# Optimization experiments

Measured on AMD Instinct MI355X. Metric: run time of the kernel, lower is better.

Reference implementation:

```python
import jax, jax.numpy as jnp
import numpy as np

B, T, D = 2, 2048, 2048
N, K, H = 16, 8, 128  # num_heads, num_kv_heads, head_dim
SOFTCAP = 50.0
ROPE_BASE = 10000.0


def apply_rope(x, positions):
    # x: [B, L, heads, H], positions: [B, L]
    head_dim = x.shape[-1]
    fraction = 2.0 * jnp.arange(head_dim // 2, dtype=jnp.float32) / head_dim
    timescale = ROPE_BASE ** fraction  # [H/2]
    sinusoid = positions.astype(jnp.float32)[..., None] / timescale  # [B, L, H/2]
    sinusoid = sinusoid[..., None, :]  # [B, L, 1, H/2]
    sin, cos = jnp.sin(sinusoid), jnp.cos(sinusoid)
    first, second = jnp.split(x, 2, axis=-1)
    out = jnp.concatenate([first * cos - second * sin,
                           second * cos + first * sin], axis=-1)
    return out.astype(x.dtype)


def setup_inputs() -> dict:
    key = jax.random.key(0)
    kx, kq, kkv, ko = jax.random.split(key, 4)
    x = jax.random.normal(kx, (B, T, D), dtype=jnp.float32)
    positions = jnp.broadcast_to(jnp.arange(T, dtype=jnp.int32), (B, T))
    attn_mask = jnp.broadcast_to(
        jnp.tril(jnp.ones((T, T), dtype=bool))[None, None], (B, 1, T, T))
    # variance-scaling fan_in init approximated with scaled normals
    w_q = jax.random.normal(kq, (N, D, H), dtype=jnp.float32) / np.sqrt(D)
    w_kv = jax.random.normal(kkv, (2, K, D, H), dtype=jnp.float32) / np.sqrt(D)
    w_out = jax.random.normal(ko, (N, H, D), dtype=jnp.float32) / np.sqrt(N * H)
    return {"x": x, "positions": positions, "attn_mask": attn_mask,
            "w_q": w_q, "w_kv": w_kv, "w_out": w_out}


def reference(x, positions, attn_mask, w_q, w_kv, w_out):
    # QKV projections (GQA: separate q and kv einsums)
    q = jnp.einsum('BTD,NDH->BTNH', x, w_q)        # [B,T,N,H]
    kv = jnp.einsum('BSD,cKDH->cBSKH', x, w_kv)     # [2,B,S,K,H]
    k, v = kv[0], kv[1]
    q = apply_rope(q, positions) * (H ** -0.5)      # rsqrt_head_dim norm
    k = apply_rope(k, positions)
    # GQA grouping: N = K * G
    G = N // K
    qg = q.reshape(B, T, K, G, H)
    logits = jnp.einsum('BTKGH,BSKH->BKGTS', qg, k).astype(jnp.float32)
    logits = jnp.tanh(logits / SOFTCAP) * SOFTCAP   # logits softcap
    big_neg = -2.3819763e+38
    masked = jnp.where(attn_mask[:, :, None, :, :], logits, big_neg)
    probs = jax.nn.softmax(masked, axis=-1).astype(k.dtype)
    encoded = jnp.einsum('BKGTS,BSKH->BTKGH', probs, v).reshape(B, T, N, H)
    return jnp.einsum('BTNH,NHD->BTD', encoded, w_out)
```

## Files before the change

kernel.cpp:

```cpp
#include <hip/hip_runtime.h>
#include <math.h>
#include <stdint.h>


typedef unsigned short u16;
using bf16x8 = __attribute__((ext_vector_type(8))) short;
using f32x4  = __attribute__((ext_vector_type(4))) float;

#define MFMA_BF16(a,b,c) __builtin_amdgcn_mfma_f32_16x16x32_bf16((a),(b),(c),0,0,0)

static __device__ __forceinline__ float b2f(u16 u) {
  union { unsigned int i; float f; } v; v.i = ((unsigned int)u) << 16; return v.f;
}
static __device__ __forceinline__ u16 f2b(float f) {
  union { float f; unsigned int i; } v; v.f = f;
  unsigned int r = v.i + 0x7fffu + ((v.i >> 16) & 1u);
  return (u16)(r >> 16);
}
static __device__ __forceinline__ unsigned pk2(float x0, float x1) {
  union { float f; unsigned u; } a, b;
  a.f = x0; b.f = x1;
  return __builtin_amdgcn_perm(b.u + 0x8000u, a.u + 0x8000u, 0x07060302u);
}
static __device__ __forceinline__ void gload_lds16(const void* g, void* l) {
  __builtin_amdgcn_global_load_lds((__attribute__((address_space(1))) void*)(g),
                                   (__attribute__((address_space(3))) void*)(l),
                                   16, 0, 0);
}

__global__ __launch_bounds__(256) void f32_to_bf16(const float* __restrict__ src,
                                                   u16* __restrict__ dst, int n) {
  const int i = (blockIdx.x * 256 + threadIdx.x) * 4;
  if (i < n) {
    const float4 v = *(const float4*)(src + i);
    ushort4 o;
    o.x = f2b(v.x); o.y = f2b(v.y); o.z = f2b(v.z); o.w = f2b(v.w);
    *(ushort4*)(dst + i) = o;
  }
}

__global__ __launch_bounds__(256) void transpose_f32_bf16(const float* __restrict__ src,
                                                          u16* __restrict__ dst,
                                                          int rows, int cols) {
  __shared__ u16 tile[32][33];
  const int c0 = blockIdx.x * 32;
  const int r0 = blockIdx.y * 32;
  const size_t matoff = (size_t)blockIdx.z * (size_t)rows * (size_t)cols;
  const float* s = src + matoff;
  u16* d = dst + matoff;
  const int tx = threadIdx.x, ty = threadIdx.y;
#pragma unroll
  for (int j = 0; j < 4; ++j)
    tile[ty + j * 8][tx] = f2b(s[(size_t)(r0 + ty + j * 8) * cols + (c0 + tx)]);
  __syncthreads();
#pragma unroll
  for (int j = 0; j < 4; ++j)
    d[(size_t)(c0 + ty + j * 8) * rows + (r0 + tx)] = tile[tx][ty + j * 8];
}

__global__ __launch_bounds__(256) void gemm_qkv(const u16* __restrict__ X,
                                                const u16* __restrict__ wqt,
                                                const u16* __restrict__ wkvt,
                                                u16* __restrict__ qb,
                                                u16* __restrict__ kb,
                                                u16* __restrict__ vtb) {
  __shared__ __align__(16) u16 sA[128 * 32];
  __shared__ __align__(16) u16 sB[128 * 32];
  const int m0 = blockIdx.x * 128;
  const int ct = blockIdx.y;
  const u16* Bt = (ct < 16) ? (wqt + (size_t)ct * 128 * 2048)
                            : (wkvt + (size_t)(ct - 16) * 128 * 2048);
  const int tid = threadIdx.x;
  const int wave = tid >> 6, lane = tid & 63;
  const int wm = wave & 1, wn = wave >> 1;
  const int quad = lane >> 4, l16 = lane & 15;
  const int srow = lane >> 2, sch = lane & 3;

  f32x4 acc[4][4] = {};

  for (int k0 = 0; k0 < 2048; k0 += 32) {
#pragma unroll
    for (int s = 0; s < 2; ++s) {
      const int instr = wave * 2 + s;
      const int row = instr * 16 + srow;
      gload_lds16(X + (size_t)(m0 + row) * 2048 + k0 + sch * 8, (char*)sA + instr * 1024);
      gload_lds16(Bt + (size_t)row * 2048 + k0 + sch * 8, (char*)sB + instr * 1024);
    }
    __syncthreads();
    bf16x8 af[4], bfr[4];
#pragma unroll
    for (int mf = 0; mf < 4; ++mf)
      af[mf] = *(const bf16x8*)(sA + (wm * 64 + mf * 16 + l16) * 32 + quad * 8);
#pragma unroll
    for (int nf = 0; nf < 4; ++nf)
      bfr[nf] = *(const bf16x8*)(sB + (wn * 64 + nf * 16 + l16) * 32 + quad * 8);
#pragma unroll
    for (int mf = 0; mf < 4; ++mf)
#pragma unroll
      for (int nf = 0; nf < 4; ++nf)
        acc[mf][nf] = MFMA_BF16(af[mf], bfr[nf], acc[mf][nf]);
    __syncthreads();
  }

#pragma unroll
  for (int mf = 0; mf < 4; ++mf) {
    const int mm = m0 + wm * 64 + mf * 16 + quad * 4;
    const int b = mm >> 11;
    const int t = mm & 2047;
#pragma unroll
    for (int nf = 0; nf < 4; ++nf) {
      const int h = wn * 64 + nf * 16 + l16;
      if (ct < 16) {
        u16* d = qb + (((size_t)b * 16 + ct) * 2048 + t) * 128 + h;
#pragma unroll
        for (int i = 0; i < 4; ++i) d[(size_t)i * 128] = f2b(acc[mf][nf][i]);
      } else if (ct < 24) {
        u16* d = kb + (((size_t)b * 8 + (ct - 16)) * 2048 + t) * 128 + h;
#pragma unroll
        for (int i = 0; i < 4; ++i) d[(size_t)i * 128] = f2b(acc[mf][nf][i]);
      } else {
        u16* d = vtb + (((size_t)b * 8 + (ct - 24)) * 128 + h) * 2048 + t;
        uint2 pkv;
        pkv.x = (unsigned)f2b(acc[mf][nf][0]) | ((unsigned)f2b(acc[mf][nf][1]) << 16);
        pkv.y = (unsigned)f2b(acc[mf][nf][2]) | ((unsigned)f2b(acc[mf][nf][3]) << 16);
        *(uint2*)d = pkv;
      }
    }
  }
}

__global__ __launch_bounds__(256) void rope_kernel(u16* __restrict__ qb,
                                                   u16* __restrict__ kb,
                                                   const int* __restrict__ pos) {
  const size_t idx = (size_t)blockIdx.x * 256 + threadIdx.x;
  const size_t QP = (size_t)1 << 22;
  u16* p;
  float scale;
  int b, t, j;
  if (idx < QP) {
    j = (int)(idx & 63); t = (int)((idx >> 6) & 2047);
    const int hd = (int)((idx >> 17) & 15); b = (int)(idx >> 21);
    p = qb + (((size_t)b * 16 + hd) * 2048 + t) * 128;
    scale = 0.08838834764831845f;
  } else {
    const size_t r = idx - QP;
    j = (int)(r & 63); t = (int)((r >> 6) & 2047);
    const int hd = (int)((r >> 17) & 7); b = (int)(r >> 20);
    p = kb + (((size_t)b * 8 + hd) * 2048 + t) * 128;
    scale = 1.0f;
  }
  const float fpos = (float)pos[(size_t)b * 2048 + t];
  const float ts = __powf(10000.0f, (float)j * (1.0f / 64.0f));
  const float ang = fpos / ts;
  float sn, cs;
  sincosf(ang, &sn, &cs);
  const float a = b2f(p[j]);
  const float c2 = b2f(p[j + 64]);
  p[j] = f2b((a * cs - c2 * sn) * scale);
  p[j + 64] = f2b((c2 * cs + a * sn) * scale);
}

__global__ __launch_bounds__(256) void attn_fused(const u16* __restrict__ qg,
                                                  const u16* __restrict__ kg,
                                                  const u16* __restrict__ vtg,
                                                  u16* __restrict__ enc) {
  __shared__ __align__(16) char lds[32768];
  char* sK = lds;
  char* sV = lds + 16384;

  const int bid = blockIdx.x;
  const int x = bid & 7;
  const int i6 = bid >> 3;
  const int p = i6 & 15;
  const int head = (i6 >> 4) * 8 + x;
  const int b = head >> 4;
  const int n = head & 15;
  const int kh = n >> 1;

  const u16* qbase = qg + ((size_t)b * 16 + n) * 2048 * 128;
  const u16* kbase = kg + ((size_t)b * 8 + kh) * 2048 * 128;
  const u16* vbase = vtg + ((size_t)b * 8 + kh) * 128 * 2048;

  const int tid = threadIdx.x, wave = tid >> 6, lane = tid & 63;
  const int quad = lane >> 4, l16 = lane & 15;
  const int bp_a0 = ((quad & 1) * 32 + l16) * 4;
  const int bp_a1 = bp_a0 + 64;

  const float L2E = 1.4426950408889634f;
  const float C50 = 72.13475204444817f;
  const float A1 = 1.3333333333e-4f;
  const float A2 = 2.1333333333e-8f;
  const float A3 = 3.4539682540e-12f;

#pragma unroll 1
  for (int pass = 0; pass < 2; ++pass) {
    const int Q = pass ? (31 - p) : p;
    const int tw = Q * 64 + wave * 16;
    const int tlane = tw + l16;

    bf16x8 qf[4];
#pragma unroll
    for (int kf = 0; kf < 4; ++kf)
      qf[kf] = *(const bf16x8*)(qbase + (size_t)tlane * 128 + kf * 32 + quad * 8);

    f32x4 o[8] = {};
    f32x4 lacc = {0.f, 0.f, 0.f, 0.f};

#pragma unroll 1
    for (int si = 0; si <= Q; ++si) {
      const int s0 = si * 64;
      __syncthreads();
#pragma unroll
      for (int r2 = 0; r2 < 4; ++r2) {
        const int idx = r2 * 256 + tid;
        const int kr = idx >> 4, kc = idx & 15;
        *(float4*)(sK + kr * 256 + ((kc ^ (kr & 15)) << 4)) =
            *(const float4*)(kbase + (size_t)(s0 + kr) * 128 + kc * 8);
        const int vr = idx >> 3, vc = idx & 7;
        *(float4*)(sV + vr * 128 + ((vc ^ (vr & 7)) << 4)) =
            *(const float4*)(vbase + (size_t)vr * 2048 + s0 + vc * 8);
      }
      __syncthreads();

      const bool diag = (si == Q);
      const int nfmax = diag ? wave : 3;
      const int kmax = diag ? (wave >> 1) : 1;

      f32x4 sacc[4];
#pragma unroll
      for (int nf = 0; nf < 4; ++nf) {
        if (nf <= nfmax) {
          const int sr = nf * 16 + l16;
          f32x4 a = {0.f, 0.f, 0.f, 0.f};
#pragma unroll
          for (int kf = 0; kf < 4; ++kf) {
            const bf16x8 kfr =
                *(const bf16x8*)(sK + sr * 256 + (((kf * 4 + quad) ^ (sr & 15)) << 4));
            a = MFMA_BF16(kfr, qf[kf], a);
          }
          sacc[nf] = a;
        }
      }

#pragma unroll
      for (int nf = 0; nf < 4; ++nf) {
        if (nf <= nfmax) {
          const f32x4 xv = sacc[nf];
          const f32x4 u = xv * xv;
          f32x4 t = u * (-A3) + A2;
          t = u * t + (-A1);
          t = u * t + 1.0f;
          const f32x4 tc = xv * t;
          f32x4 pv;
#pragma unroll
          for (int i = 0; i < 4; ++i) pv[i] = exp2f(fmaf(tc[i], L2E, -C50));
          if (diag) {
#pragma unroll
            for (int i = 0; i < 4; ++i) {
              const int sg = s0 + nf * 16 + quad * 4 + i;
              if (sg > tlane) pv[i] = 0.0f;
            }
          }
          sacc[nf] = pv;
          lacc += pv;
        }
      }

      unsigned pkd[4][2];
#pragma unroll
      for (int nf = 0; nf < 4; ++nf) {
        if (nf <= nfmax) {
          pkd[nf][0] = pk2(sacc[nf][0], sacc[nf][1]);
          pkd[nf][1] = pk2(sacc[nf][2], sacc[nf][3]);
        } else {
          pkd[nf][0] = 0u; pkd[nf][1] = 0u;
        }
      }

#pragma unroll
      for (int c2 = 0; c2 < 2; ++c2) {
        if (c2 <= kmax) {
          const int lo = (quad >> 1);
          const int dA0 = __builtin_amdgcn_ds_bpermute(bp_a0, (int)pkd[2 * c2][0]);
          const int dB0 = __builtin_amdgcn_ds_bpermute(bp_a0, (int)pkd[2 * c2 + 1][0]);
          const int dA1 = __builtin_amdgcn_ds_bpermute(bp_a0, (int)pkd[2 * c2][1]);
          const int dB1 = __builtin_amdgcn_ds_bpermute(bp_a0, (int)pkd[2 * c2 + 1][1]);
          const int dA2 = __builtin_amdgcn_ds_bpermute(bp_a1, (int)pkd[2 * c2][0]);
          const int dB2 = __builtin_amdgcn_ds_bpermute(bp_a1, (int)pkd[2 * c2 + 1][0]);
          const int dA3 = __builtin_amdgcn_ds_bpermute(bp_a1, (int)pkd[2 * c2][1]);
          const int dB3 = __builtin_amdgcn_ds_bpermute(bp_a1, (int)pkd[2 * c2 + 1][1]);
          union { int d[4]; bf16x8 v; } pb;
          pb.d[0] = lo ? dB0 : dA0;
          pb.d[1] = lo ? dB1 : dA1;
          pb.d[2] = lo ? dB2 : dA2;
          pb.d[3] = lo ? dB3 : dA3;
#pragma unroll
          for (int nfo = 0; nfo < 8; ++nfo) {
            const int hr = nfo * 16 + l16;
            const bf16x8 vb =
                *(const bf16x8*)(sV + hr * 128 + (((c2 * 4 + quad) ^ (hr & 7)) << 4));
            o[nfo] = MFMA_BF16(vb, pb.v, o[nfo]);
          }
        }
      }
    }

    float lsum = lacc[0] + lacc[1] + lacc[2] + lacc[3];
    lsum += __shfl_xor(lsum, 16);
    lsum += __shfl_xor(lsum, 32);
    const float inv = 1.0f / lsum;
    u16* d = enc + (((size_t)b * 2048 + tlane) * 16 + n) * 128 + quad * 4;
#pragma unroll
    for (int nfo = 0; nfo < 8; ++nfo) {
      uint2 st;
      st.x = (unsigned)f2b(o[nfo][0] * inv) | ((unsigned)f2b(o[nfo][1] * inv) << 16);
      st.y = (unsigned)f2b(o[nfo][2] * inv) | ((unsigned)f2b(o[nfo][3] * inv) << 16);
      *(uint2*)(d + nfo * 16) = st;
    }
  }
}

__global__ __launch_bounds__(256) void gemm_out(const u16* __restrict__ A,
                                                const u16* __restrict__ Bt,
                                                float* __restrict__ C) {
  __shared__ __align__(16) u16 sA[128 * 32];
  __shared__ __align__(16) u16 sB[128 * 32];
  const int m0 = blockIdx.x * 128;
  const int n0 = blockIdx.y * 128;
  const int tid = threadIdx.x;
  const int wave = tid >> 6, lane = tid & 63;
  const int wm = wave & 1, wn = wave >> 1;
  const int quad = lane >> 4, l16 = lane & 15;
  const int srow = lane >> 2, sch = lane & 3;

  f32x4 acc[4][4] = {};

  for (int k0 = 0; k0 < 2048; k0 += 32) {
#pragma unroll
    for (int s = 0; s < 2; ++s) {
      const int instr = wave * 2 + s;
      const int row = instr * 16 + srow;
      gload_lds16(A + (size_t)(m0 + row) * 2048 + k0 + sch * 8, (char*)sA + instr * 1024);
      gload_lds16(Bt + (size_t)(n0 + row) * 2048 + k0 + sch * 8, (char*)sB + instr * 1024);
    }
    __syncthreads();
    bf16x8 af[4], bfr[4];
#pragma unroll
    for (int mf = 0; mf < 4; ++mf)
      af[mf] = *(const bf16x8*)(sA + (wm * 64 + mf * 16 + l16) * 32 + quad * 8);
#pragma unroll
    for (int nf = 0; nf < 4; ++nf)
      bfr[nf] = *(const bf16x8*)(sB + (wn * 64 + nf * 16 + l16) * 32 + quad * 8);
#pragma unroll
    for (int mf = 0; mf < 4; ++mf)
#pragma unroll
      for (int nf = 0; nf < 4; ++nf)
        acc[mf][nf] = MFMA_BF16(af[mf], bfr[nf], acc[mf][nf]);
    __syncthreads();
  }

#pragma unroll
  for (int mf = 0; mf < 4; ++mf) {
    const int mm = m0 + wm * 64 + mf * 16 + quad * 4;
#pragma unroll
    for (int nf = 0; nf < 4; ++nf) {
      const int col = n0 + wn * 64 + nf * 16 + l16;
#pragma unroll
      for (int i = 0; i < 4; ++i) C[(size_t)(mm + i) * 2048 + col] = acc[mf][nf][i];
    }
  }
}

extern "C" void kernel_launch(void* const* d_in, const int* in_sizes, int n_in,
                              void* d_out, int out_size, void* d_ws, size_t ws_size,
                              hipStream_t stream) {
  (void)in_sizes; (void)n_in; (void)out_size; (void)ws_size;
  const float* x     = (const float*)d_in[0];
  const int*   posi  = (const int*)d_in[1];
  const float* w_q   = (const float*)d_in[3];
  const float* w_kv  = (const float*)d_in[4];
  const float* w_out = (const float*)d_in[5];
  float* out = (float*)d_out;

  u16* ws = (u16*)d_ws;
  u16* wqt   = ws;
  u16* wkvt  = ws + (size_t)4194304;
  u16* woutt = ws + (size_t)8388608;
  u16* qb    = ws + (size_t)12582912;
  u16* kb    = ws + (size_t)20971520;
  u16* vtb   = ws + (size_t)25165824;
  u16* encb  = ws + (size_t)29360128;
  u16* xb    = encb;

  f32_to_bf16<<<8192, 256, 0, stream>>>(x, xb, 8388608);
  transpose_f32_bf16<<<dim3(4, 64, 16), dim3(32, 8, 1), 0, stream>>>(w_q, wqt, 2048, 128);
  transpose_f32_bf16<<<dim3(4, 64, 16), dim3(32, 8, 1), 0, stream>>>(w_kv, wkvt, 2048, 128);
  transpose_f32_bf16<<<dim3(64, 64, 1), dim3(32, 8, 1), 0, stream>>>(w_out, woutt, 2048, 2048);
  gemm_qkv<<<dim3(32, 32), 256, 0, stream>>>(xb, wqt, wkvt, qb, kb, vtb);
  rope_kernel<<<24576, 256, 0, stream>>>(qb, kb, posi);
  attn_fused<<<512, 256, 0, stream>>>(qb, kb, vtb, encb);
  gemm_out<<<dim3(32, 16), 256, 0, stream>>>(encb, woutt, out);
}
```

Baseline: 407.3 us.

## Fuse prep kernels, deepen GEMM K-tile with XOR-swizzled LDS, vectorize RoPE

Merges the input conversion and the three weight transposes into one prep launch, which removes three kernel launches. Both GEMMs now stage a 64-wide K slice per iteration, with an XOR swizzle on the LDS chunk index to avoid bank conflicts. This halves the number of barriers per K loop and doubles LDS use per block. RoPE now handles two element pairs per thread with 32-bit loads and stores, halving the thread count.

```diff
diff --git a/kernel.cpp b/kernel.cpp
--- a/kernel.cpp
+++ b/kernel.cpp
@@ -28,77 +28,101 @@
                                    16, 0, 0);
 }
 
-__global__ __launch_bounds__(256) void f32_to_bf16(const float* __restrict__ src,
-                                                   u16* __restrict__ dst, int n) {
-  const int i = (blockIdx.x * 256 + threadIdx.x) * 4;
-  if (i < n) {
-    const float4 v = *(const float4*)(src + i);
+__global__ __launch_bounds__(256) void prep(const float* __restrict__ x, u16* __restrict__ xb,
+                                            const float* __restrict__ wq,
+                                            const float* __restrict__ wkv,
+                                            const float* __restrict__ wout,
+                                            u16* __restrict__ wqkvt, u16* __restrict__ woutt) {
+  const int tid = threadIdx.x;
+  int bid = blockIdx.x;
+  if (bid < 8192) {
+    const int i = (bid * 256 + tid) * 4;
+    const float4 v = *(const float4*)(x + i);
     ushort4 o;
     o.x = f2b(v.x); o.y = f2b(v.y); o.z = f2b(v.z); o.w = f2b(v.w);
-    *(ushort4*)(dst + i) = o;
-  }
-}
-
-__global__ __launch_bounds__(256) void transpose_f32_bf16(const float* __restrict__ src,
-                                                          u16* __restrict__ dst,
-                                                          int rows, int cols) {
+    *(ushort4*)(xb + i) = o;
+    return;
+  }
+  bid -= 8192;
+  const float* src;
+  u16* dst;
+  int rows, cols, bx, by;
+  if (bid < 8192) {
+    const int seg = bid >> 12;
+    const int r = bid & 4095;
+    const int mat = r >> 8;
+    bx = (r & 255) & 3;
+    by = (r & 255) >> 2;
+    rows = 2048; cols = 128;
+    src = (seg ? wkv : wq) + (size_t)mat * 2048 * 128;
+    dst = wqkvt + (size_t)(seg * 16 + mat) * 2048 * 128;
+  } else {
+    const int r = bid - 8192;
+    bx = r & 63;
+    by = r >> 6;
+    rows = 2048; cols = 2048;
+    src = wout;
+    dst = woutt;
+  }
   __shared__ u16 tile[32][33];
-  const int c0 = blockIdx.x * 32;
-  const int r0 = blockIdx.y * 32;
-  const size_t matoff = (size_t)blockIdx.z * (size_t)rows * (size_t)cols;
-  const float* s = src + matoff;
-  u16* d = dst + matoff;
-  const int tx = threadIdx.x, ty = threadIdx.y;
+  const int c0 = bx * 32, r0 = by * 32;
+  const int tx = tid & 31, ty = tid >> 5;
 #pragma unroll
   for (int j = 0; j < 4; ++j)
-    tile[ty + j * 8][tx] = f2b(s[(size_t)(r0 + ty + j * 8) * cols + (c0 + tx)]);
+    tile[ty + j * 8][tx] = f2b(src[(size_t)(r0 + ty + j * 8) * cols + (c0 + tx)]);
   __syncthreads();
 #pragma unroll
   for (int j = 0; j < 4; ++j)
-    d[(size_t)(c0 + ty + j * 8) * rows + (r0 + tx)] = tile[tx][ty + j * 8];
+    dst[(size_t)(c0 + ty + j * 8) * rows + (r0 + tx)] = tile[tx][ty + j * 8];
 }
 
 __global__ __launch_bounds__(256) void gemm_qkv(const u16* __restrict__ X,
-                                                const u16* __restrict__ wqt,
-                                                const u16* __restrict__ wkvt,
+                                                const u16* __restrict__ wqkvt,
                                                 u16* __restrict__ qb,
                                                 u16* __restrict__ kb,
                                                 u16* __restrict__ vtb) {
-  __shared__ __align__(16) u16 sA[128 * 32];
-  __shared__ __align__(16) u16 sB[128 * 32];
+  __shared__ __align__(16) u16 sA[128 * 64];
+  __shared__ __align__(16) u16 sB[128 * 64];
   const int m0 = blockIdx.x * 128;
   const int ct = blockIdx.y;
-  const u16* Bt = (ct < 16) ? (wqt + (size_t)ct * 128 * 2048)
-                            : (wkvt + (size_t)(ct - 16) * 128 * 2048);
+  const u16* Bt = wqkvt + (size_t)ct * 128 * 2048;
   const int tid = threadIdx.x;
   const int wave = tid >> 6, lane = tid & 63;
   const int wm = wave & 1, wn = wave >> 1;
   const int quad = lane >> 4, l16 = lane & 15;
-  const int srow = lane >> 2, sch = lane & 3;
+  const int srow = lane >> 3;
+  const int sch = (lane & 7) ^ srow;
 
   f32x4 acc[4][4] = {};
 
-  for (int k0 = 0; k0 < 2048; k0 += 32) {
-#pragma unroll
-    for (int s = 0; s < 2; ++s) {
-      const int instr = wave * 2 + s;
-      const int row = instr * 16 + srow;
+  for (int k0 = 0; k0 < 2048; k0 += 64) {
+#pragma unroll
+    for (int s = 0; s < 4; ++s) {
+      const int instr = wave * 4 + s;
+      const int row = instr * 8 + srow;
       gload_lds16(X + (size_t)(m0 + row) * 2048 + k0 + sch * 8, (char*)sA + instr * 1024);
       gload_lds16(Bt + (size_t)row * 2048 + k0 + sch * 8, (char*)sB + instr * 1024);
     }
     __syncthreads();
-    bf16x8 af[4], bfr[4];
-#pragma unroll
-    for (int mf = 0; mf < 4; ++mf)
-      af[mf] = *(const bf16x8*)(sA + (wm * 64 + mf * 16 + l16) * 32 + quad * 8);
-#pragma unroll
-    for (int nf = 0; nf < 4; ++nf)
-      bfr[nf] = *(const bf16x8*)(sB + (wn * 64 + nf * 16 + l16) * 32 + quad * 8);
-#pragma unroll
-    for (int mf = 0; mf < 4; ++mf)
-#pragma unroll
-      for (int nf = 0; nf < 4; ++nf)
-        acc[mf][nf] = MFMA_BF16(af[mf], bfr[nf], acc[mf][nf]);
+#pragma unroll
+    for (int ks = 0; ks < 2; ++ks) {
+      bf16x8 af[4], bfr[4];
+#pragma unroll
+      for (int mf = 0; mf < 4; ++mf) {
+        const int R = wm * 64 + mf * 16 + l16;
+        af[mf] = *(const bf16x8*)((char*)sA + R * 128 + (((ks * 4 + quad) ^ (R & 7)) << 4));
+      }
+#pragma unroll
+      for (int nf = 0; nf < 4; ++nf) {
+        const int R = wn * 64 + nf * 16 + l16;
+        bfr[nf] = *(const bf16x8*)((char*)sB + R * 128 + (((ks * 4 + quad) ^ (R & 7)) << 4));
+      }
+#pragma unroll
+      for (int mf = 0; mf < 4; ++mf)
+#pragma unroll
+        for (int nf = 0; nf < 4; ++nf)
+          acc[mf][nf] = MFMA_BF16(af[mf], bfr[nf], acc[mf][nf]);
+    }
     __syncthreads();
   }
 
@@ -132,32 +156,40 @@
 __global__ __launch_bounds__(256) void rope_kernel(u16* __restrict__ qb,
                                                    u16* __restrict__ kb,
                                                    const int* __restrict__ pos) {
-  const size_t idx = (size_t)blockIdx.x * 256 + threadIdx.x;
-  const size_t QP = (size_t)1 << 22;
+  const unsigned idx = blockIdx.x * 256 + threadIdx.x;
+  const unsigned QP = 1u << 21;
   u16* p;
   float scale;
-  int b, t, j;
+  int b, t, j2;
   if (idx < QP) {
-    j = (int)(idx & 63); t = (int)((idx >> 6) & 2047);
-    const int hd = (int)((idx >> 17) & 15); b = (int)(idx >> 21);
+    j2 = (int)(idx & 31) * 2; t = (int)((idx >> 5) & 2047);
+    const int hd = (int)((idx >> 16) & 15); b = (int)(idx >> 20);
     p = qb + (((size_t)b * 16 + hd) * 2048 + t) * 128;
     scale = 0.08838834764831845f;
   } else {
-    const size_t r = idx - QP;
-    j = (int)(r & 63); t = (int)((r >> 6) & 2047);
-    const int hd = (int)((r >> 17) & 7); b = (int)(r >> 20);
+    const unsigned r = idx - QP;
+    j2 = (int)(r & 31) * 2; t = (int)((r >> 5) & 2047);
+    const int hd = (int)((r >> 16) & 7); b = (int)(r >> 19);
     p = kb + (((size_t)b * 8 + hd) * 2048 + t) * 128;
     scale = 1.0f;
   }
   const float fpos = (float)pos[(size_t)b * 2048 + t];
-  const float ts = __powf(10000.0f, (float)j * (1.0f / 64.0f));
-  const float ang = fpos / ts;
-  float sn, cs;
-  sincosf(ang, &sn, &cs);
-  const float a = b2f(p[j]);
-  const float c2 = b2f(p[j + 64]);
-  p[j] = f2b((a * cs - c2 * sn) * scale);
-  p[j + 64] = f2b((c2 * cs + a * sn) * scale);
+  const unsigned lo = *(const unsigned*)(p + j2);
+  const unsigned hi = *(const unsigned*)(p + j2 + 64);
+  unsigned olo = 0, ohi = 0;
+#pragma unroll
+  for (int d = 0; d < 2; ++d) {
+    const int j = j2 + d;
+    const float ts = __powf(10000.0f, (float)j * (1.0f / 64.0f));
+    float sn, cs;
+    sincosf(fpos / ts, &sn, &cs);
+    const float a = b2f((u16)((d ? (lo >> 16) : lo) & 0xffffu));
+    const float c2 = b2f((u16)((d ? (hi >> 16) : hi) & 0xffffu));
+    olo |= ((unsigned)f2b((a * cs - c2 * sn) * scale)) << (16 * d);
+    ohi |= ((unsigned)f2b((c2 * cs + a * sn) * scale)) << (16 * d);
+  }
+  *(unsigned*)(p + j2) = olo;
+  *(unsigned*)(p + j2 + 64) = ohi;
 }
 
 __global__ __launch_bounds__(256) void attn_fused(const u16* __restrict__ qg,
@@ -323,39 +355,47 @@
 __global__ __launch_bounds__(256) void gemm_out(const u16* __restrict__ A,
                                                 const u16* __restrict__ Bt,
                                                 float* __restrict__ C) {
-  __shared__ __align__(16) u16 sA[128 * 32];
-  __shared__ __align__(16) u16 sB[128 * 32];
+  __shared__ __align__(16) u16 sA[128 * 64];
+  __shared__ __align__(16) u16 sB[128 * 64];
   const int m0 = blockIdx.x * 128;
   const int n0 = blockIdx.y * 128;
   const int tid = threadIdx.x;
   const int wave = tid >> 6, lane = tid & 63;
   const int wm = wave & 1, wn = wave >> 1;
   const int quad = lane >> 4, l16 = lane & 15;
-  const int srow = lane >> 2, sch = lane & 3;
+  const int srow = lane >> 3;
+  const int sch = (lane & 7) ^ srow;
 
   f32x4 acc[4][4] = {};
 
-  for (int k0 = 0; k0 < 2048; k0 += 32) {
-#pragma unroll
-    for (int s = 0; s < 2; ++s) {
-      const int instr = wave * 2 + s;
-      const int row = instr * 16 + srow;
+  for (int k0 = 0; k0 < 2048; k0 += 64) {
+#pragma unroll
+    for (int s = 0; s < 4; ++s) {
+      const int instr = wave * 4 + s;
+      const int row = instr * 8 + srow;
       gload_lds16(A + (size_t)(m0 + row) * 2048 + k0 + sch * 8, (char*)sA + instr * 1024);
       gload_lds16(Bt + (size_t)(n0 + row) * 2048 + k0 + sch * 8, (char*)sB + instr * 1024);
     }
     __syncthreads();
-    bf16x8 af[4], bfr[4];
-#pragma unroll
-    for (int mf = 0; mf < 4; ++mf)
-      af[mf] = *(const bf16x8*)(sA + (wm * 64 + mf * 16 + l16) * 32 + quad * 8);
-#pragma unroll
-    for (int nf = 0; nf < 4; ++nf)
-      bfr[nf] = *(const bf16x8*)(sB + (wn * 64 + nf * 16 + l16) * 32 + quad * 8);
-#pragma unroll
-    for (int mf = 0; mf < 4; ++mf)
-#pragma unroll
-      for (int nf = 0; nf < 4; ++nf)
-        acc[mf][nf] = MFMA_BF16(af[mf], bfr[nf], acc[mf][nf]);
+#pragma unroll
+    for (int ks = 0; ks < 2; ++ks) {
+      bf16x8 af[4], bfr[4];
+#pragma unroll
+      for (int mf = 0; mf < 4; ++mf) {
+        const int R = wm * 64 + mf * 16 + l16;
+        af[mf] = *(const bf16x8*)((char*)sA + R * 128 + (((ks * 4 + quad) ^ (R & 7)) << 4));
+      }
+#pragma unroll
+      for (int nf = 0; nf < 4; ++nf) {
+        const int R = wn * 64 + nf * 16 + l16;
+        bfr[nf] = *(const bf16x8*)((char*)sB + R * 128 + (((ks * 4 + quad) ^ (R & 7)) << 4));
+      }
+#pragma unroll
+      for (int mf = 0; mf < 4; ++mf)
+#pragma unroll
+        for (int nf = 0; nf < 4; ++nf)
+          acc[mf][nf] = MFMA_BF16(af[mf], bfr[nf], acc[mf][nf]);
+    }
     __syncthreads();
   }
 
@@ -383,8 +423,7 @@
   float* out = (float*)d_out;
 
   u16* ws = (u16*)d_ws;
-  u16* wqt   = ws;
-  u16* wkvt  = ws + (size_t)4194304;
+  u16* wqkvt = ws;
   u16* woutt = ws + (size_t)8388608;
   u16* qb    = ws + (size_t)12582912;
   u16* kb    = ws + (size_t)20971520;
@@ -392,12 +431,9 @@
   u16* encb  = ws + (size_t)29360128;
   u16* xb    = encb;
 
-  f32_to_bf16<<<8192, 256, 0, stream>>>(x, xb, 8388608);
-  transpose_f32_bf16<<<dim3(4, 64, 16), dim3(32, 8, 1), 0, stream>>>(w_q, wqt, 2048, 128);
-  transpose_f32_bf16<<<dim3(4, 64, 16), dim3(32, 8, 1), 0, stream>>>(w_kv, wkvt, 2048, 128);
-  transpose_f32_bf16<<<dim3(64, 64, 1), dim3(32, 8, 1), 0, stream>>>(w_out, woutt, 2048, 2048);
-  gemm_qkv<<<dim3(32, 32), 256, 0, stream>>>(xb, wqt, wkvt, qb, kb, vtb);
-  rope_kernel<<<24576, 256, 0, stream>>>(qb, kb, posi);
+  prep<<<20480, 256, 0, stream>>>(x, xb, w_q, w_kv, w_out, wqkvt, woutt);
+  gemm_qkv<<<dim3(32, 32), 256, 0, stream>>>(xb, wqkvt, qb, kb, vtb);
+  rope_kernel<<<12288, 256, 0, stream>>>(qb, kb, posi);
   attn_fused<<<512, 256, 0, stream>>>(qb, kb, vtb, encb);
   gemm_out<<<dim3(32, 16), 256, 0, stream>>>(encb, woutt, out);
 }
```

Result: faster. 395.8 us (-2.8%).
